# Performance work log

Hardware: AMD Instinct MI355X
Metric: run time of the kernel (lower is better)

The kernel has to match this reference:

```python
import jax, jax.numpy as jnp
import numpy as np

B, T, D, H, FF, TB = 4, 512, 768, 12, 3072, 64
DK = D // H
E = float(np.e)
NEG = -1e9  # stand-in for float('-inf') masked_fill; rows always have valid entries


def layer_norm(x, g, b, eps=1e-5):
    m = jnp.mean(x, axis=-1, keepdims=True)
    v = jnp.mean((x - m) ** 2, axis=-1, keepdims=True)
    return (x - m) * jax.lax.rsqrt(v + eps) * g + b


def setup_inputs() -> dict:
    key = jax.random.key(0)
    ks = jax.random.split(key, 20)
    s = 0.02
    w = lambda k, shape: jax.random.normal(k, shape, jnp.float32) * s
    return {
        "x": jax.random.normal(ks[0], (B, T, D), jnp.float32),
        "batch_temporal_mat": jax.random.uniform(ks[1], (B, T, T), jnp.float32, 0.0, 100.0),
        "padding_masks": jnp.ones((B, 1, T, T), jnp.int32),
        # attention linears (stored (in,out): y = x @ W + b, equals torch x @ W_t.T + b)
        "wq": w(ks[2], (D, D)), "bq": w(ks[3], (D,)),
        "wk": w(ks[4], (D, D)), "bk": w(ks[5], (D,)),
        "wv": w(ks[6], (D, D)), "bv": w(ks[7], (D,)),
        "wp": w(ks[8], (D, D)), "bp": w(ks[9], (D,)),
        # temporal-bias MLP: Linear(1,TB) -> leaky_relu(0.2) -> Linear(TB,1)
        "tb1_w": w(ks[10], (1, TB)), "tb1_b": w(ks[11], (TB,)),
        "tb2_w": w(ks[12], (TB, 1)), "tb2_b": w(ks[13], (1,)),
        # FFN
        "fc1_w": w(ks[14], (D, FF)), "fc1_b": w(ks[15], (FF,)),
        "fc2_w": w(ks[16], (FF, D)), "fc2_b": w(ks[17], (D,)),
        # layernorms
        "ln1_g": jnp.ones((D,), jnp.float32), "ln1_b": jnp.zeros((D,), jnp.float32),
        "ln2_g": jnp.ones((D,), jnp.float32), "ln2_b": jnp.zeros((D,), jnp.float32),
    }


def _block(x, batch_temporal_mat, padding_masks,
           wq, bq, wk, bk, wv, bv, wp, bp,
           tb1_w, tb1_b, tb2_w, tb2_b,
           fc1_w, fc1_b, fc2_w, fc2_b,
           ln1_g, ln1_b, ln2_g, ln2_b):
    # pre-LN attention sublayer
    h = layer_norm(x, ln1_g, ln1_b)
    q = (h @ wq + bq).reshape(B, T, H, DK).transpose(0, 2, 1, 3)  # (B,H,T,DK)
    k = (h @ wk + bk).reshape(B, T, H, DK).transpose(0, 2, 1, 3)
    v = (h @ wv + bv).reshape(B, T, H, DK).transpose(0, 2, 1, 3)
    scores = jnp.einsum('bhid,bhjd->bhij', q, k) * (DK ** -0.5)  # (B,H,T,T)

    # temporal bias: 1/log(e + dt), then per-(i,j) MLP with leaky_relu(0.2)
    tm = 1.0 / jnp.log(E + batch_temporal_mat)                    # (B,T,T)
    hb = jax.nn.leaky_relu(tm[..., None] @ tb1_w + tb1_b, 0.2)    # (B,T,T,TB)
    bias = (hb @ tb2_w + tb2_b)[..., 0]                           # (B,T,T)
    scores = scores + bias[:, None]

    # padding mask then causal (future) mask with CLS row 0 fully visible
    scores = jnp.where(padding_masks == 0, NEG, scores)
    causal = jnp.triu(jnp.ones((T, T), bool), 1).at[0, :].set(False)
    scores = jnp.where(causal, NEG, scores)

    p = jax.nn.softmax(scores, axis=-1)
    out = jnp.einsum('bhij,bhjd->bhid', p, v).transpose(0, 2, 1, 3).reshape(B, T, D)
    out = out @ wp + bp
    x = x + out

    # pre-LN FFN sublayer (exact GELU as in nn.GELU default)
    h2 = layer_norm(x, ln2_g, ln2_b)
    m = jax.nn.gelu(h2 @ fc1_w + fc1_b, approximate=False) @ fc2_w + fc2_b
    return x + m


def reference(x, batch_temporal_mat, padding_masks,
              wq, bq, wk, bk, wv, bv, wp, bp,
              tb1_w, tb1_b, tb2_w, tb2_b,
              fc1_w, fc1_b, fc2_w, fc2_b,
              ln1_g, ln1_b, ln2_g, ln2_b):
    return _block(x, batch_temporal_mat, padding_masks,
                  wq, bq, wk, bk, wv, bv, wp, bp,
                  tb1_w, tb1_b, tb2_w, tb2_b,
                  fc1_w, fc1_b, fc2_w, fc2_b,
                  ln1_g, ln1_b, ln2_g, ln2_b)
```

## Files before the change

### kernel.cpp

```cpp
#include <hip/hip_runtime.h>
#include <hip/hip_bf16.h>
#include <math.h>

#define B_ 4
#define T_ 512
#define D_ 768
#define H_ 12
#define FF_ 3072
#define DK_ 64
#define NTOK (B_*T_)
#define NEGV -1e9f

typedef unsigned short u16;
typedef __bf16 bfx8 __attribute__((ext_vector_type(8)));
typedef float f32x4 __attribute__((ext_vector_type(4)));
typedef u16 u16x8 __attribute__((ext_vector_type(8)));

__device__ __forceinline__ u16 f2bf(float f) {
  union { float f; unsigned u; } v; v.f = f;
  unsigned r = (v.u + 0x7FFFu + ((v.u >> 16) & 1u)) >> 16;
  return (u16)r;
}

__device__ __forceinline__ void glds16(const u16* g, u16* l) {
  __builtin_amdgcn_global_load_lds((const __attribute__((address_space(1))) void*)g,
                                   (__attribute__((address_space(3))) void*)l, 16, 0, 0);
}

__global__ void transpose_all(const float* __restrict__ wq, const float* __restrict__ wk,
                              const float* __restrict__ wv, const float* __restrict__ wp,
                              const float* __restrict__ fc1, const float* __restrict__ fc2,
                              u16* wqT, u16* wkT, u16* wvT, u16* wpT, u16* fc1T, u16* fc2T)
{
  __shared__ float tile[32][33];
  const int bid = blockIdx.x;
  const float* in; u16* outp; int K, N, local;
  if (bid < 2304) {
    int m = bid / 576; local = bid % 576; K = 768; N = 768;
    in   = m == 0 ? wq  : (m == 1 ? wk  : (m == 2 ? wv  : wp));
    outp = m == 0 ? wqT : (m == 1 ? wkT : (m == 2 ? wvT : wpT));
  } else if (bid < 4608) {
    local = bid - 2304; K = 768; N = 3072; in = fc1; outp = fc1T;
  } else {
    local = bid - 4608; K = 3072; N = 768; in = fc2; outp = fc2T;
  }
  const int nt = N / 32;
  const int n0 = (local % nt) * 32, k0 = (local / nt) * 32;
  const int tx = threadIdx.x, ty = threadIdx.y;
  #pragma unroll
  for (int i = 0; i < 4; ++i) {
    int r = ty + i * 8;
    tile[r][tx] = in[(size_t)(k0 + r) * N + n0 + tx];
  }
  __syncthreads();
  #pragma unroll
  for (int i = 0; i < 4; ++i) {
    int r = ty + i * 8;
    outp[(size_t)(n0 + r) * K + k0 + tx] = f2bf(tile[tx][r]);
  }
}

__global__ __launch_bounds__(256) void ln_cast(const float* __restrict__ x, const float* __restrict__ g,
                                               const float* __restrict__ b, u16* __restrict__ out)
{
  const int row = blockIdx.x;
  const int tid = threadIdx.x;
  const float* xr = x + (size_t)row * D_;
  float v0 = xr[tid], v1 = xr[tid + 256], v2 = xr[tid + 512];
  float s = v0 + v1 + v2;
  float sq = v0 * v0 + v1 * v1 + v2 * v2;
  #pragma unroll
  for (int o = 32; o > 0; o >>= 1) { s += __shfl_down(s, o); sq += __shfl_down(sq, o); }
  __shared__ float ss[4], s2[4];
  int w = tid >> 6;
  if ((tid & 63) == 0) { ss[w] = s; s2[w] = sq; }
  __syncthreads();
  s = ss[0] + ss[1] + ss[2] + ss[3];
  sq = s2[0] + s2[1] + s2[2] + s2[3];
  float mean = s * (1.0f / 768.0f);
  float inv = rsqrtf(sq * (1.0f / 768.0f) - mean * mean + 1e-5f);
  u16* orow = out + (size_t)row * D_;
  orow[tid]       = f2bf((v0 - mean) * inv * g[tid]       + b[tid]);
  orow[tid + 256] = f2bf((v1 - mean) * inv * g[tid + 256] + b[tid + 256]);
  orow[tid + 512] = f2bf((v2 - mean) * inv * g[tid + 512] + b[tid + 512]);
}

__global__ __launch_bounds__(256) void bias_mlp(const float* __restrict__ tmat, const int* __restrict__ pad,
    const float* __restrict__ w1, const float* __restrict__ b1,
    const float* __restrict__ w2, const float* __restrict__ b2,
    float* __restrict__ biasM)
{
  __shared__ float sw1[64], sb1[64], sw2[64];
  if (threadIdx.x < 64) {
    sw1[threadIdx.x] = w1[threadIdx.x];
    sb1[threadIdx.x] = b1[threadIdx.x];
    sw2[threadIdx.x] = w2[threadIdx.x];
  }
  __syncthreads();
  size_t idx = (size_t)blockIdx.x * 256 + threadIdx.x;
  float tm = 1.0f / __logf(2.718281828459045f + tmat[idx]);
  float acc = b2[0];
  #pragma unroll
  for (int t = 0; t < 64; ++t) {
    float u = fmaf(tm, sw1[t], sb1[t]);
    u = u > 0.0f ? u : 0.2f * u;
    acc = fmaf(u, sw2[t], acc);
  }
  biasM[idx] = (pad[idx] == 0) ? NEGV : acc;
}

__device__ __forceinline__ void gemm_tile_db(
    const u16* __restrict__ A, const u16* __restrict__ BT,
    int K, int nk, int m0, int n0, int k0,
    u16* As, u16* Bs, f32x4 acc[4][4])
{
  const int tid = threadIdx.x;
  const int w = tid >> 6, lane = tid & 63;
  const int lr = lane & 15, lk = (lane >> 4) * 8;
  const int wm = (w >> 1) * 64, wn = (w & 1) * 64;
  const int c0 = w * 64 + lane, c1 = 256 + c0;
  const int r0 = c0 >> 2, o0 = (c0 & 3) * 8;
  const int r1 = c1 >> 2, o1 = (c1 & 3) * 8;
  const u16* ga0 = A  + (size_t)(m0 + r0) * K + k0 + o0;
  const u16* ga1 = A  + (size_t)(m0 + r1) * K + k0 + o1;
  const u16* gb0 = BT + (size_t)(n0 + r0) * K + k0 + o0;
  const u16* gb1 = BT + (size_t)(n0 + r1) * K + k0 + o1;
  u16* la0 = As + w * 512;
  u16* la1 = As + 2048 + w * 512;
  u16* lb0 = Bs + w * 512;
  u16* lb1 = Bs + 2048 + w * 512;
  glds16(ga0, la0); glds16(ga1, la1); glds16(gb0, lb0); glds16(gb1, lb1);
  __syncthreads();
  int cur = 0;
  for (int kt = 0; kt < nk; ++kt) {
    const int nxt = cur ^ 1;
    if (kt + 1 < nk) {
      ga0 += 32; ga1 += 32; gb0 += 32; gb1 += 32;
      glds16(ga0, la0 + nxt * 4096); glds16(ga1, la1 + nxt * 4096);
      glds16(gb0, lb0 + nxt * 4096); glds16(gb1, lb1 + nxt * 4096);
    }
    const u16* Asc = As + cur * 4096;
    const u16* Bsc = Bs + cur * 4096;
    bfx8 af[4], bfr[4];
    #pragma unroll
    for (int t = 0; t < 4; ++t) {
      af[t]  = *(const bfx8*)&Asc[(wm + t * 16 + lr) * 32 + lk];
      bfr[t] = *(const bfx8*)&Bsc[(wn + t * 16 + lr) * 32 + lk];
    }
    #pragma unroll
    for (int rt = 0; rt < 4; ++rt)
      #pragma unroll
      for (int ct = 0; ct < 4; ++ct)
        acc[rt][ct] = __builtin_amdgcn_mfma_f32_16x16x32_bf16(af[rt], bfr[ct], acc[rt][ct], 0, 0, 0);
    __syncthreads();
    cur = nxt;
  }
}

__global__ __launch_bounds__(256) void gemm_qkv(
    const u16* __restrict__ A,
    const u16* __restrict__ wqT, const u16* __restrict__ wkT, const u16* __restrict__ wvT,
    const float* __restrict__ bq, const float* __restrict__ bk, const float* __restrict__ bv,
    u16* __restrict__ qo, u16* __restrict__ ko, u16* __restrict__ vo)
{
  __shared__ u16 As[2 * 128 * 32];
  __shared__ u16 Bs[2 * 128 * 32];
  const int z = blockIdx.z;
  const u16* BT = z == 0 ? wqT : (z == 1 ? wkT : wvT);
  const float* bias = z == 0 ? bq : (z == 1 ? bk : bv);
  u16* outp = z == 0 ? qo : (z == 1 ? ko : vo);
  const float scale = z == 0 ? 0.125f : 1.0f;
  const int m0 = blockIdx.y * 128, n0 = blockIdx.x * 128;
  f32x4 acc[4][4];
  #pragma unroll
  for (int a = 0; a < 4; ++a)
    #pragma unroll
    for (int bb = 0; bb < 4; ++bb) acc[a][bb] = (f32x4){0.f, 0.f, 0.f, 0.f};
  gemm_tile_db(A, BT, D_, D_ / 32, m0, n0, 0, As, Bs, acc);
  const int tid = threadIdx.x;
  const int w = tid >> 6, lane = tid & 63;
  const int lr = lane & 15;
  const int wm = (w >> 1) * 64, wn = (w & 1) * 64;
  #pragma unroll
  for (int rt = 0; rt < 4; ++rt)
    #pragma unroll
    for (int ct = 0; ct < 4; ++ct)
      #pragma unroll
      for (int r = 0; r < 4; ++r) {
        int m = m0 + wm + rt * 16 + (lane >> 4) * 4 + r;
        int n = n0 + wn + ct * 16 + lr;
        float val = (acc[rt][ct][r] + bias[n]) * scale;
        int b = m >> 9, t = m & 511, hh = n >> 6, d = n & 63;
        if (z < 2) outp[(((size_t)b * H_ + hh) * T_ + t) * DK_ + d] = f2bf(val);
        else       outp[(((size_t)b * H_ + hh) * DK_ + d) * T_ + t] = f2bf(val);
      }
}

__global__ __launch_bounds__(256) void gemm_part(
    const u16* __restrict__ A, const u16* __restrict__ BT,
    float* __restrict__ part, int M, int N, int K, int Ksplit)
{
  __shared__ u16 As[2 * 128 * 32];
  __shared__ u16 Bs[2 * 128 * 32];
  const int m0 = blockIdx.y * 128, n0 = blockIdx.x * 128;
  const int kz = blockIdx.z;
  f32x4 acc[4][4];
  #pragma unroll
  for (int a = 0; a < 4; ++a)
    #pragma unroll
    for (int bb = 0; bb < 4; ++bb) acc[a][bb] = (f32x4){0.f, 0.f, 0.f, 0.f};
  gemm_tile_db(A, BT, K, Ksplit / 32, m0, n0, kz * Ksplit, As, Bs, acc);
  const int tid = threadIdx.x;
  const int w = tid >> 6, lane = tid & 63;
  const int lr = lane & 15;
  const int wm = (w >> 1) * 64, wn = (w & 1) * 64;
  float* pp = part + (size_t)kz * M * N;
  #pragma unroll
  for (int rt = 0; rt < 4; ++rt)
    #pragma unroll
    for (int ct = 0; ct < 4; ++ct)
      #pragma unroll
      for (int r = 0; r < 4; ++r) {
        int m = m0 + wm + rt * 16 + (lane >> 4) * 4 + r;
        int n = n0 + wn + ct * 16 + lr;
        pp[(size_t)m * N + n] = acc[rt][ct][r];
      }
}

__global__ __launch_bounds__(256) void gemm_gelu(
    const u16* __restrict__ A, const u16* __restrict__ BT,
    const float* __restrict__ bias, u16* __restrict__ outp, int M, int N, int K)
{
  __shared__ u16 As[2 * 128 * 32];
  __shared__ u16 Bs[2 * 128 * 32];
  const int m0 = blockIdx.y * 128, n0 = blockIdx.x * 128;
  f32x4 acc[4][4];
  #pragma unroll
  for (int a = 0; a < 4; ++a)
    #pragma unroll
    for (int bb = 0; bb < 4; ++bb) acc[a][bb] = (f32x4){0.f, 0.f, 0.f, 0.f};
  gemm_tile_db(A, BT, K, K / 32, m0, n0, 0, As, Bs, acc);
  const int tid = threadIdx.x;
  const int w = tid >> 6, lane = tid & 63;
  const int lr = lane & 15;
  const int wm = (w >> 1) * 64, wn = (w & 1) * 64;
  #pragma unroll
  for (int rt = 0; rt < 4; ++rt)
    #pragma unroll
    for (int ct = 0; ct < 4; ++ct)
      #pragma unroll
      for (int r = 0; r < 4; ++r) {
        int m = m0 + wm + rt * 16 + (lane >> 4) * 4 + r;
        int n = n0 + wn + ct * 16 + lr;
        float val = acc[rt][ct][r] + bias[n];
        float gl = 0.5f * val * (1.0f + erff(val * 0.7071067811865475f));
        outp[(size_t)m * N + n] = f2bf(gl);
      }
}

__global__ __launch_bounds__(256) void reduce_ln(
    const float* __restrict__ part, const float* __restrict__ x, const float* __restrict__ bp,
    const float* __restrict__ g, const float* __restrict__ bta,
    float* __restrict__ x1, u16* __restrict__ h2)
{
  const int row = blockIdx.x;
  const int tid = threadIdx.x;
  const size_t base = (size_t)row * D_;
  const size_t slab = (size_t)NTOK * D_;
  float v[3];
  float s = 0.f, sq = 0.f;
  #pragma unroll
  for (int i = 0; i < 3; ++i) {
    int c = tid + i * 256;
    float val = x[base + c] + bp[c] + part[base + c] + part[slab + base + c];
    v[i] = val;
    s += val; sq += val * val;
  }
  #pragma unroll
  for (int o = 32; o > 0; o >>= 1) { s += __shfl_down(s, o); sq += __shfl_down(sq, o); }
  __shared__ float ss[4], s2[4];
  int w = tid >> 6;
  if ((tid & 63) == 0) { ss[w] = s; s2[w] = sq; }
  __syncthreads();
  s = ss[0] + ss[1] + ss[2] + ss[3];
  sq = s2[0] + s2[1] + s2[2] + s2[3];
  float mean = s * (1.0f / 768.0f);
  float inv = rsqrtf(sq * (1.0f / 768.0f) - mean * mean + 1e-5f);
  #pragma unroll
  for (int i = 0; i < 3; ++i) {
    int c = tid + i * 256;
    x1[base + c] = v[i];
    h2[base + c] = f2bf((v[i] - mean) * inv * g[c] + bta[c]);
  }
}

__global__ __launch_bounds__(256) void reduce_out(
    const float* __restrict__ part, const float* __restrict__ x1,
    const float* __restrict__ bias, float* __restrict__ out)
{
  const size_t i = (size_t)blockIdx.x * 256 + threadIdx.x;
  const size_t slab = (size_t)NTOK * D_ / 4;
  float4 b = ((const float4*)bias)[i % (D_ / 4)];
  float4 a = ((const float4*)x1)[i];
  float4 p0 = ((const float4*)part)[i];
  float4 p1 = ((const float4*)part)[i + slab];
  float4 p2 = ((const float4*)part)[i + 2 * slab];
  float4 p3 = ((const float4*)part)[i + 3 * slab];
  float4 o;
  o.x = a.x + b.x + p0.x + p1.x + p2.x + p3.x;
  o.y = a.y + b.y + p0.y + p1.y + p2.y + p3.y;
  o.z = a.z + b.z + p0.z + p1.z + p2.z + p3.z;
  o.w = a.w + b.w + p0.w + p1.w + p2.w + p3.w;
  ((float4*)out)[i] = o;
}

__global__ __launch_bounds__(256) void attn_kernel(
    const u16* __restrict__ q, const u16* __restrict__ k, const u16* __restrict__ vT,
    const float* __restrict__ biasM, u16* __restrict__ ao)
{
  __shared__ u16 P[16 * 512];
  __shared__ float pmax[64], psum[64];
  const int tid = threadIdx.x;
  const int w = tid >> 6, lane = tid & 63;
  const int lr = lane & 15, hi = lane >> 4, lk = hi * 8;

  const int bid = blockIdx.x;
  const int xcd = bid & 7, idx = bid >> 3;
  const int bh = xcd * 6 + (idx >> 5);
  const int i0 = (idx & 31) * 16;
  const int b = bh / H_, h = bh % H_;
  const int tmax = (i0 == 0) ? 31 : ((i0 >> 4) + 1);
  const int nks  = (i0 == 0) ? 16 : ((i0 >> 5) + 1);

  bfx8 qf[2];
  #pragma unroll
  for (int ks = 0; ks < 2; ++ks)
    qf[ks] = *(const bfx8*)(q + ((size_t)bh * T_ + i0 + lr) * DK_ + ks * 32 + lk);
  f32x4 acc[8];
  float mx[4] = {-3.4e38f, -3.4e38f, -3.4e38f, -3.4e38f};
  #pragma unroll
  for (int ct = 0; ct < 8; ++ct) {
    const int t = ct * 4 + w;
    if (t > tmax) continue;
    const int j0 = t * 16;
    bfx8 kf0 = *(const bfx8*)(k + ((size_t)bh * T_ + j0 + lr) * DK_ + lk);
    bfx8 kf1 = *(const bfx8*)(k + ((size_t)bh * T_ + j0 + lr) * DK_ + 32 + lk);
    f32x4 a0 = (f32x4){0.f, 0.f, 0.f, 0.f};
    a0 = __builtin_amdgcn_mfma_f32_16x16x32_bf16(qf[0], kf0, a0, 0, 0, 0);
    a0 = __builtin_amdgcn_mfma_f32_16x16x32_bf16(qf[1], kf1, a0, 0, 0, 0);
    const int j = j0 + lr;
    #pragma unroll
    for (int r = 0; r < 4; ++r) {
      int i = i0 + hi * 4 + r;
      float s = a0[r] + biasM[((size_t)b * T_ + i) * T_ + j];
      if (j > i && i != 0) s = NEGV;
      a0[r] = s;
      mx[r] = fmaxf(mx[r], s);
    }
    acc[ct] = a0;
  }
  #pragma unroll
  for (int o = 1; o < 16; o <<= 1)
    #pragma unroll
    for (int r = 0; r < 4; ++r) mx[r] = fmaxf(mx[r], __shfl_xor(mx[r], o));
  if (lr == 0) {
    #pragma unroll
    for (int r = 0; r < 4; ++r) pmax[w * 16 + hi * 4 + r] = mx[r];
  }
  __syncthreads();

  float sm[4] = {0.f, 0.f, 0.f, 0.f};
  float M[4];
  #pragma unroll
  for (int r = 0; r < 4; ++r) {
    int row = hi * 4 + r;
    M[r] = fmaxf(fmaxf(pmax[row], pmax[16 + row]), fmaxf(pmax[32 + row], pmax[48 + row]));
  }
  char* Pb = (char*)P;
  #pragma unroll
  for (int ct = 0; ct < 8; ++ct) {
    const int t = ct * 4 + w;
    if (t > tmax) continue;
    const int col = t * 16 + lr;
    #pragma unroll
    for (int r = 0; r < 4; ++r) {
      float p = __expf(acc[ct][r] - M[r]);
      sm[r] += p;
      int row = hi * 4 + r;
      int byte = (row * 1024 + col * 2) ^ ((row & 7) << 4);
      *(u16*)(Pb + byte) = f2bf(p);
    }
  }
  #pragma unroll
  for (int o = 1; o < 16; o <<= 1)
    #pragma unroll
    for (int r = 0; r < 4; ++r) sm[r] += __shfl_xor(sm[r], o);
  if (lr == 0) {
    #pragma unroll
    for (int r = 0; r < 4; ++r) psum[w * 16 + hi * 4 + r] = sm[r];
  }
  __syncthreads();

  float rinv[4];
  #pragma unroll
  for (int r = 0; r < 4; ++r) {
    int row = hi * 4 + r;
    rinv[r] = 1.0f / (psum[row] + psum[16 + row] + psum[32 + row] + psum[48 + row]);
  }

  {
    const int n0 = w * 16;
    f32x4 oacc = (f32x4){0.f, 0.f, 0.f, 0.f};
    for (int ks = 0; ks < nks; ++ks) {
      int byte = (lr * 1024 + (ks * 32 + lk) * 2) ^ ((lr & 7) << 4);
      bfx8 pa = *(const bfx8*)(Pb + byte);
      bfx8 vf = *(const bfx8*)(vT + ((size_t)bh * DK_ + n0 + lr) * T_ + ks * 32 + lk);
      oacc = __builtin_amdgcn_mfma_f32_16x16x32_bf16(pa, vf, oacc, 0, 0, 0);
    }
    #pragma unroll
    for (int r = 0; r < 4; ++r) {
      int i = i0 + hi * 4 + r;
      ao[((size_t)b * T_ + i) * D_ + h * DK_ + n0 + lr] = f2bf(oacc[r] * rinv[r]);
    }
  }
}

extern "C" void kernel_launch(void* const* d_in, const int* in_sizes, int n_in,
                              void* d_out, int out_size, void* d_ws, size_t ws_size,
                              hipStream_t stream) {
  (void)in_sizes; (void)n_in; (void)out_size; (void)ws_size;
  const float* x    = (const float*)d_in[0];
  const float* tmat = (const float*)d_in[1];
  const int*   pad  = (const int*)d_in[2];
  const float* wq = (const float*)d_in[3];  const float* bq = (const float*)d_in[4];
  const float* wk = (const float*)d_in[5];  const float* bk = (const float*)d_in[6];
  const float* wv = (const float*)d_in[7];  const float* bv = (const float*)d_in[8];
  const float* wp = (const float*)d_in[9];  const float* bp = (const float*)d_in[10];
  const float* tb1w = (const float*)d_in[11]; const float* tb1b = (const float*)d_in[12];
  const float* tb2w = (const float*)d_in[13]; const float* tb2b = (const float*)d_in[14];
  const float* fc1w = (const float*)d_in[15]; const float* fc1b = (const float*)d_in[16];
  const float* fc2w = (const float*)d_in[17]; const float* fc2b = (const float*)d_in[18];
  const float* ln1g = (const float*)d_in[19]; const float* ln1b = (const float*)d_in[20];
  const float* ln2g = (const float*)d_in[21]; const float* ln2b = (const float*)d_in[22];
  float* out = (float*)d_out;

  char* p = (char*)d_ws;
  u16* wqT  = (u16*)p; p += (size_t)768 * 768 * 2;
  u16* wkT  = (u16*)p; p += (size_t)768 * 768 * 2;
  u16* wvT  = (u16*)p; p += (size_t)768 * 768 * 2;
  u16* wpT  = (u16*)p; p += (size_t)768 * 768 * 2;
  u16* fc1T = (u16*)p; p += (size_t)768 * 3072 * 2;
  u16* fc2T = (u16*)p; p += (size_t)3072 * 768 * 2;
  float* x1 = (float*)p; p += (size_t)NTOK * D_ * 4;
  u16* gbuf = (u16*)p; p += (size_t)NTOK * FF_ * 2;
  char* pool = p;
  u16*   hbuf  = (u16*)(pool + 0);
  u16*   qb    = (u16*)(pool + 3145728);
  u16*   kb    = (u16*)(pool + 6291456);
  u16*   vTb   = (u16*)(pool + 9437184);
  float* biasM = (float*)(pool + 12582912);
  u16*   ao    = (u16*)(pool + 16777216);
  u16*   h2    = (u16*)(pool + 19922944);
  float* partP = (float*)(pool + 0);
  float* partF = (float*)(pool + 0);

  transpose_all<<<6912, dim3(32, 8), 0, stream>>>(wq, wk, wv, wp, fc1w, fc2w,
                                                  wqT, wkT, wvT, wpT, fc1T, fc2T);
  ln_cast<<<NTOK, 256, 0, stream>>>(x, ln1g, ln1b, hbuf);
  bias_mlp<<<(B_ * T_ * T_) / 256, 256, 0, stream>>>(tmat, pad, tb1w, tb1b, tb2w, tb2b, biasM);

  gemm_qkv<<<dim3(6, 16, 3), 256, 0, stream>>>(hbuf, wqT, wkT, wvT, bq, bk, bv, qb, kb, vTb);
  attn_kernel<<<1536, 256, 0, stream>>>(qb, kb, vTb, biasM, ao);

  gemm_part<<<dim3(6, 16, 2), 256, 0, stream>>>(ao, wpT, partP, NTOK, 768, 768, 384);
  reduce_ln<<<NTOK, 256, 0, stream>>>(partP, x, bp, ln2g, ln2b, x1, h2);

  gemm_gelu<<<dim3(24, 16), 256, 0, stream>>>(h2, fc1T, fc1b, gbuf, NTOK, FF_, 768);

  gemm_part<<<dim3(6, 16, 4), 256, 0, stream>>>(gbuf, fc2T, partF, NTOK, 768, 3072, 768);
  reduce_out<<<NTOK * D_ / 4 / 256, 256, 0, stream>>>(partF, x1, fc2b, out);
}
```

Before: 153.1 us.

## Merge prep kernels, triple-buffer GEMM loads, and process 32 query rows per attention block

Combines the weight transpose, LN1 cast and temporal-bias MLP into a single launch. Replaces the double-buffered GEMM K-loop with a three-stage ring that keeps two tiles in flight, using explicit vmcnt waits and one barrier per iteration. Changes the attention kernel so each block handles 32 query rows instead of 16, reusing the K and V fragments across two row groups and halving the grid. This raises LDS use and register pressure, which may reduce occupancy.

```diff
diff --git a/kernel.cpp b/kernel.cpp
--- a/kernel.cpp
+++ b/kernel.cpp
@@ -27,89 +27,88 @@
                                    (__attribute__((address_space(3))) void*)l, 16, 0, 0);
 }
 
-__global__ void transpose_all(const float* __restrict__ wq, const float* __restrict__ wk,
-                              const float* __restrict__ wv, const float* __restrict__ wp,
-                              const float* __restrict__ fc1, const float* __restrict__ fc2,
-                              u16* wqT, u16* wkT, u16* wvT, u16* wpT, u16* fc1T, u16* fc2T)
-{
-  __shared__ float tile[32][33];
+__global__ __launch_bounds__(256) void prep_kernel(
+    const float* __restrict__ x,
+    const float* __restrict__ wq, const float* __restrict__ wk,
+    const float* __restrict__ wv, const float* __restrict__ wp,
+    const float* __restrict__ fc1, const float* __restrict__ fc2,
+    u16* wqT, u16* wkT, u16* wvT, u16* wpT, u16* fc1T, u16* fc2T,
+    const float* __restrict__ ln1g, const float* __restrict__ ln1b, u16* __restrict__ hbuf,
+    const float* __restrict__ tmat, const int* __restrict__ pad,
+    const float* __restrict__ tb1w, const float* __restrict__ tb1b,
+    const float* __restrict__ tb2w, const float* __restrict__ tb2b,
+    float* __restrict__ biasM)
+{
   const int bid = blockIdx.x;
-  const float* in; u16* outp; int K, N, local;
-  if (bid < 2304) {
-    int m = bid / 576; local = bid % 576; K = 768; N = 768;
-    in   = m == 0 ? wq  : (m == 1 ? wk  : (m == 2 ? wv  : wp));
-    outp = m == 0 ? wqT : (m == 1 ? wkT : (m == 2 ? wvT : wpT));
-  } else if (bid < 4608) {
-    local = bid - 2304; K = 768; N = 3072; in = fc1; outp = fc1T;
+  const int tid = threadIdx.x;
+  if (bid < 6912) {
+    __shared__ float tile[32][33];
+    const float* in; u16* outp; int K, N, local;
+    if (bid < 2304) {
+      int m = bid / 576; local = bid % 576; K = 768; N = 768;
+      in   = m == 0 ? wq  : (m == 1 ? wk  : (m == 2 ? wv  : wp));
+      outp = m == 0 ? wqT : (m == 1 ? wkT : (m == 2 ? wvT : wpT));
+    } else if (bid < 4608) {
+      local = bid - 2304; K = 768; N = 3072; in = fc1; outp = fc1T;
+    } else {
+      local = bid - 4608; K = 3072; N = 768; in = fc2; outp = fc2T;
+    }
+    const int nt = N / 32;
+    const int n0 = (local % nt) * 32, k0 = (local / nt) * 32;
+    const int tx = tid & 31, ty = tid >> 5;
+    #pragma unroll
+    for (int i = 0; i < 4; ++i) {
+      int r = ty + i * 8;
+      tile[r][tx] = in[(size_t)(k0 + r) * N + n0 + tx];
+    }
+    __syncthreads();
+    #pragma unroll
+    for (int i = 0; i < 4; ++i) {
+      int r = ty + i * 8;
+      outp[(size_t)(n0 + r) * K + k0 + tx] = f2bf(tile[tx][r]);
+    }
+  } else if (bid < 8960) {
+    const int row = bid - 6912;
+    const float* xr = x + (size_t)row * D_;
+    float v0 = xr[tid], v1 = xr[tid + 256], v2 = xr[tid + 512];
+    float s = v0 + v1 + v2;
+    float sq = v0 * v0 + v1 * v1 + v2 * v2;
+    #pragma unroll
+    for (int o = 32; o > 0; o >>= 1) { s += __shfl_down(s, o); sq += __shfl_down(sq, o); }
+    __shared__ float ss[4], s2[4];
+    int w = tid >> 6;
+    if ((tid & 63) == 0) { ss[w] = s; s2[w] = sq; }
+    __syncthreads();
+    s = ss[0] + ss[1] + ss[2] + ss[3];
+    sq = s2[0] + s2[1] + s2[2] + s2[3];
+    float mean = s * (1.0f / 768.0f);
+    float inv = rsqrtf(sq * (1.0f / 768.0f) - mean * mean + 1e-5f);
+    u16* orow = hbuf + (size_t)row * D_;
+    orow[tid]       = f2bf((v0 - mean) * inv * ln1g[tid]       + ln1b[tid]);
+    orow[tid + 256] = f2bf((v1 - mean) * inv * ln1g[tid + 256] + ln1b[tid + 256]);
+    orow[tid + 512] = f2bf((v2 - mean) * inv * ln1g[tid + 512] + ln1b[tid + 512]);
   } else {
-    local = bid - 4608; K = 3072; N = 768; in = fc2; outp = fc2T;
-  }
-  const int nt = N / 32;
-  const int n0 = (local % nt) * 32, k0 = (local / nt) * 32;
-  const int tx = threadIdx.x, ty = threadIdx.y;
-  #pragma unroll
-  for (int i = 0; i < 4; ++i) {
-    int r = ty + i * 8;
-    tile[r][tx] = in[(size_t)(k0 + r) * N + n0 + tx];
-  }
-  __syncthreads();
-  #pragma unroll
-  for (int i = 0; i < 4; ++i) {
-    int r = ty + i * 8;
-    outp[(size_t)(n0 + r) * K + k0 + tx] = f2bf(tile[tx][r]);
-  }
-}
-
-__global__ __launch_bounds__(256) void ln_cast(const float* __restrict__ x, const float* __restrict__ g,
-                                               const float* __restrict__ b, u16* __restrict__ out)
-{
-  const int row = blockIdx.x;
-  const int tid = threadIdx.x;
-  const float* xr = x + (size_t)row * D_;
-  float v0 = xr[tid], v1 = xr[tid + 256], v2 = xr[tid + 512];
-  float s = v0 + v1 + v2;
-  float sq = v0 * v0 + v1 * v1 + v2 * v2;
-  #pragma unroll
-  for (int o = 32; o > 0; o >>= 1) { s += __shfl_down(s, o); sq += __shfl_down(sq, o); }
-  __shared__ float ss[4], s2[4];
-  int w = tid >> 6;
-  if ((tid & 63) == 0) { ss[w] = s; s2[w] = sq; }
-  __syncthreads();
-  s = ss[0] + ss[1] + ss[2] + ss[3];
-  sq = s2[0] + s2[1] + s2[2] + s2[3];
-  float mean = s * (1.0f / 768.0f);
-  float inv = rsqrtf(sq * (1.0f / 768.0f) - mean * mean + 1e-5f);
-  u16* orow = out + (size_t)row * D_;
-  orow[tid]       = f2bf((v0 - mean) * inv * g[tid]       + b[tid]);
-  orow[tid + 256] = f2bf((v1 - mean) * inv * g[tid + 256] + b[tid + 256]);
-  orow[tid + 512] = f2bf((v2 - mean) * inv * g[tid + 512] + b[tid + 512]);
-}
-
-__global__ __launch_bounds__(256) void bias_mlp(const float* __restrict__ tmat, const int* __restrict__ pad,
-    const float* __restrict__ w1, const float* __restrict__ b1,
-    const float* __restrict__ w2, const float* __restrict__ b2,
-    float* __restrict__ biasM)
-{
-  __shared__ float sw1[64], sb1[64], sw2[64];
-  if (threadIdx.x < 64) {
-    sw1[threadIdx.x] = w1[threadIdx.x];
-    sb1[threadIdx.x] = b1[threadIdx.x];
-    sw2[threadIdx.x] = w2[threadIdx.x];
-  }
-  __syncthreads();
-  size_t idx = (size_t)blockIdx.x * 256 + threadIdx.x;
-  float tm = 1.0f / __logf(2.718281828459045f + tmat[idx]);
-  float acc = b2[0];
-  #pragma unroll
-  for (int t = 0; t < 64; ++t) {
-    float u = fmaf(tm, sw1[t], sb1[t]);
-    u = u > 0.0f ? u : 0.2f * u;
-    acc = fmaf(u, sw2[t], acc);
-  }
-  biasM[idx] = (pad[idx] == 0) ? NEGV : acc;
-}
-
-__device__ __forceinline__ void gemm_tile_db(
+    __shared__ float sw1[64], sb1[64], sw2[64];
+    if (tid < 64) {
+      sw1[tid] = tb1w[tid];
+      sb1[tid] = tb1b[tid];
+      sw2[tid] = tb2w[tid];
+    }
+    __syncthreads();
+    size_t idx = (size_t)(bid - 8960) * 256 + tid;
+    float tm = 1.0f / __logf(2.718281828459045f + tmat[idx]);
+    float acc = tb2b[0];
+    #pragma unroll
+    for (int t = 0; t < 64; ++t) {
+      float u = fmaf(tm, sw1[t], sb1[t]);
+      u = u > 0.0f ? u : 0.2f * u;
+      acc = fmaf(u, sw2[t], acc);
+    }
+    biasM[idx] = (pad[idx] == 0) ? NEGV : acc;
+  }
+}
+
+__device__ __forceinline__ void gemm_tile_p2(
     const u16* __restrict__ A, const u16* __restrict__ BT,
     int K, int nk, int m0, int n0, int k0,
     u16* As, u16* Bs, f32x4 acc[4][4])
@@ -121,26 +120,30 @@
   const int c0 = w * 64 + lane, c1 = 256 + c0;
   const int r0 = c0 >> 2, o0 = (c0 & 3) * 8;
   const int r1 = c1 >> 2, o1 = (c1 & 3) * 8;
-  const u16* ga0 = A  + (size_t)(m0 + r0) * K + k0 + o0;
-  const u16* ga1 = A  + (size_t)(m0 + r1) * K + k0 + o1;
-  const u16* gb0 = BT + (size_t)(n0 + r0) * K + k0 + o0;
-  const u16* gb1 = BT + (size_t)(n0 + r1) * K + k0 + o1;
+  const u16* gA0 = A  + (size_t)(m0 + r0) * K + k0 + o0;
+  const u16* gA1 = A  + (size_t)(m0 + r1) * K + k0 + o1;
+  const u16* gB0 = BT + (size_t)(n0 + r0) * K + k0 + o0;
+  const u16* gB1 = BT + (size_t)(n0 + r1) * K + k0 + o1;
   u16* la0 = As + w * 512;
   u16* la1 = As + 2048 + w * 512;
   u16* lb0 = Bs + w * 512;
   u16* lb1 = Bs + 2048 + w * 512;
-  glds16(ga0, la0); glds16(ga1, la1); glds16(gb0, lb0); glds16(gb1, lb1);
-  __syncthreads();
-  int cur = 0;
+#define ISSUE_TILE(kk, b) do { \
+    glds16(gA0 + (size_t)(kk) * 32, la0 + (b) * 4096); \
+    glds16(gA1 + (size_t)(kk) * 32, la1 + (b) * 4096); \
+    glds16(gB0 + (size_t)(kk) * 32, lb0 + (b) * 4096); \
+    glds16(gB1 + (size_t)(kk) * 32, lb1 + (b) * 4096); } while (0)
+  ISSUE_TILE(0, 0);
+  if (nk > 1) ISSUE_TILE(1, 1);
+  int cb = 0;
   for (int kt = 0; kt < nk; ++kt) {
-    const int nxt = cur ^ 1;
-    if (kt + 1 < nk) {
-      ga0 += 32; ga1 += 32; gb0 += 32; gb1 += 32;
-      glds16(ga0, la0 + nxt * 4096); glds16(ga1, la1 + nxt * 4096);
-      glds16(gb0, lb0 + nxt * 4096); glds16(gb1, lb1 + nxt * 4096);
-    }
-    const u16* Asc = As + cur * 4096;
-    const u16* Bsc = Bs + cur * 4096;
+    if (kt < nk - 2) asm volatile("s_waitcnt vmcnt(4)" ::: "memory");
+    else             asm volatile("s_waitcnt vmcnt(0)" ::: "memory");
+    __builtin_amdgcn_sched_barrier(0);
+    __builtin_amdgcn_s_barrier();
+    __builtin_amdgcn_sched_barrier(0);
+    const u16* Asc = As + cb * 4096;
+    const u16* Bsc = Bs + cb * 4096;
     bfx8 af[4], bfr[4];
     #pragma unroll
     for (int t = 0; t < 4; ++t) {
@@ -152,9 +155,13 @@
       #pragma unroll
       for (int ct = 0; ct < 4; ++ct)
         acc[rt][ct] = __builtin_amdgcn_mfma_f32_16x16x32_bf16(af[rt], bfr[ct], acc[rt][ct], 0, 0, 0);
-    __syncthreads();
-    cur = nxt;
-  }
+    if (kt + 2 < nk) {
+      int nb = cb + 2; if (nb >= 3) nb -= 3;
+      ISSUE_TILE(kt + 2, nb);
+    }
+    cb = cb + 1; if (cb >= 3) cb = 0;
+  }
+#undef ISSUE_TILE
 }
 
 __global__ __launch_bounds__(256) void gemm_qkv(
@@ -163,8 +170,8 @@
     const float* __restrict__ bq, const float* __restrict__ bk, const float* __restrict__ bv,
     u16* __restrict__ qo, u16* __restrict__ ko, u16* __restrict__ vo)
 {
-  __shared__ u16 As[2 * 128 * 32];
-  __shared__ u16 Bs[2 * 128 * 32];
+  __shared__ u16 As[3 * 128 * 32];
+  __shared__ u16 Bs[3 * 128 * 32];
   const int z = blockIdx.z;
   const u16* BT = z == 0 ? wqT : (z == 1 ? wkT : wvT);
   const float* bias = z == 0 ? bq : (z == 1 ? bk : bv);
@@ -176,7 +183,7 @@
   for (int a = 0; a < 4; ++a)
     #pragma unroll
     for (int bb = 0; bb < 4; ++bb) acc[a][bb] = (f32x4){0.f, 0.f, 0.f, 0.f};
-  gemm_tile_db(A, BT, D_, D_ / 32, m0, n0, 0, As, Bs, acc);
+  gemm_tile_p2(A, BT, D_, D_ / 32, m0, n0, 0, As, Bs, acc);
   const int tid = threadIdx.x;
   const int w = tid >> 6, lane = tid & 63;
   const int lr = lane & 15;
@@ -200,8 +207,8 @@
     const u16* __restrict__ A, const u16* __restrict__ BT,
     float* __restrict__ part, int M, int N, int K, int Ksplit)
 {
-  __shared__ u16 As[2 * 128 * 32];
-  __shared__ u16 Bs[2 * 128 * 32];
+  __shared__ u16 As[3 * 128 * 32];
+  __shared__ u16 Bs[3 * 128 * 32];
   const int m0 = blockIdx.y * 128, n0 = blockIdx.x * 128;
   const int kz = blockIdx.z;
   f32x4 acc[4][4];
@@ -209,7 +216,7 @@
   for (int a = 0; a < 4; ++a)
     #pragma unroll
     for (int bb = 0; bb < 4; ++bb) acc[a][bb] = (f32x4){0.f, 0.f, 0.f, 0.f};
-  gemm_tile_db(A, BT, K, Ksplit / 32, m0, n0, kz * Ksplit, As, Bs, acc);
+  gemm_tile_p2(A, BT, K, Ksplit / 32, m0, n0, kz * Ksplit, As, Bs, acc);
   const int tid = threadIdx.x;
   const int w = tid >> 6, lane = tid & 63;
   const int lr = lane & 15;
@@ -231,15 +238,15 @@
     const u16* __restrict__ A, const u16* __restrict__ BT,
     const float* __restrict__ bias, u16* __restrict__ outp, int M, int N, int K)
 {
-  __shared__ u16 As[2 * 128 * 32];
-  __shared__ u16 Bs[2 * 128 * 32];
+  __shared__ u16 As[3 * 128 * 32];
+  __shared__ u16 Bs[3 * 128 * 32];
   const int m0 = blockIdx.y * 128, n0 = blockIdx.x * 128;
   f32x4 acc[4][4];
   #pragma unroll
   for (int a = 0; a < 4; ++a)
     #pragma unroll
     for (int bb = 0; bb < 4; ++bb) acc[a][bb] = (f32x4){0.f, 0.f, 0.f, 0.f};
-  gemm_tile_db(A, BT, K, K / 32, m0, n0, 0, As, Bs, acc);
+  gemm_tile_p2(A, BT, K, K / 32, m0, n0, 0, As, Bs, acc);
   const int tid = threadIdx.x;
   const int w = tid >> 6, lane = tid & 63;
   const int lr = lane & 15;
@@ -318,26 +325,32 @@
     const u16* __restrict__ q, const u16* __restrict__ k, const u16* __restrict__ vT,
     const float* __restrict__ biasM, u16* __restrict__ ao)
 {
-  __shared__ u16 P[16 * 512];
-  __shared__ float pmax[64], psum[64];
+  __shared__ u16 P[32 * 512];
+  __shared__ float pmax[128], psum[128];
   const int tid = threadIdx.x;
   const int w = tid >> 6, lane = tid & 63;
   const int lr = lane & 15, hi = lane >> 4, lk = hi * 8;
 
   const int bid = blockIdx.x;
   const int xcd = bid & 7, idx = bid >> 3;
-  const int bh = xcd * 6 + (idx >> 5);
-  const int i0 = (idx & 31) * 16;
+  const int bh = xcd * 6 + (idx >> 4);
+  const int i0 = (idx & 15) * 32;
   const int b = bh / H_, h = bh % H_;
   const int tmax = (i0 == 0) ? 31 : ((i0 >> 4) + 1);
   const int nks  = (i0 == 0) ? 16 : ((i0 >> 5) + 1);
 
-  bfx8 qf[2];
-  #pragma unroll
-  for (int ks = 0; ks < 2; ++ks)
-    qf[ks] = *(const bfx8*)(q + ((size_t)bh * T_ + i0 + lr) * DK_ + ks * 32 + lk);
-  f32x4 acc[8];
-  float mx[4] = {-3.4e38f, -3.4e38f, -3.4e38f, -3.4e38f};
+  bfx8 qf[2][2];
+  #pragma unroll
+  for (int g = 0; g < 2; ++g)
+    #pragma unroll
+    for (int ks = 0; ks < 2; ++ks)
+      qf[g][ks] = *(const bfx8*)(q + ((size_t)bh * T_ + i0 + g * 16 + lr) * DK_ + ks * 32 + lk);
+  f32x4 acc[8][2];
+  float mx[2][4];
+  #pragma unroll
+  for (int g = 0; g < 2; ++g)
+    #pragma unroll
+    for (int r = 0; r < 4; ++r) mx[g][r] = -3.4e38f;
   #pragma unroll
   for (int ct = 0; ct < 8; ++ct) {
     const int t = ct * 4 + w;
@@ -345,37 +358,46 @@
     const int j0 = t * 16;
     bfx8 kf0 = *(const bfx8*)(k + ((size_t)bh * T_ + j0 + lr) * DK_ + lk);
     bfx8 kf1 = *(const bfx8*)(k + ((size_t)bh * T_ + j0 + lr) * DK_ + 32 + lk);
-    f32x4 a0 = (f32x4){0.f, 0.f, 0.f, 0.f};
-    a0 = __builtin_amdgcn_mfma_f32_16x16x32_bf16(qf[0], kf0, a0, 0, 0, 0);
-    a0 = __builtin_amdgcn_mfma_f32_16x16x32_bf16(qf[1], kf1, a0, 0, 0, 0);
     const int j = j0 + lr;
     #pragma unroll
+    for (int g = 0; g < 2; ++g) {
+      f32x4 a0 = (f32x4){0.f, 0.f, 0.f, 0.f};
+      a0 = __builtin_amdgcn_mfma_f32_16x16x32_bf16(qf[g][0], kf0, a0, 0, 0, 0);
+      a0 = __builtin_amdgcn_mfma_f32_16x16x32_bf16(qf[g][1], kf1, a0, 0, 0, 0);
+      #pragma unroll
+      for (int r = 0; r < 4; ++r) {
+        int i = i0 + g * 16 + hi * 4 + r;
+        float s = a0[r] + biasM[((size_t)b * T_ + i) * T_ + j];
+        if (j > i && i != 0) s = NEGV;
+        a0[r] = s;
+        mx[g][r] = fmaxf(mx[g][r], s);
+      }
+      acc[ct][g] = a0;
+    }
+  }
+  #pragma unroll
+  for (int o = 1; o < 16; o <<= 1)
+    #pragma unroll
+    for (int g = 0; g < 2; ++g)
+      #pragma unroll
+      for (int r = 0; r < 4; ++r) mx[g][r] = fmaxf(mx[g][r], __shfl_xor(mx[g][r], o));
+  if (lr == 0) {
+    #pragma unroll
+    for (int g = 0; g < 2; ++g)
+      #pragma unroll
+      for (int r = 0; r < 4; ++r) pmax[w * 32 + g * 16 + hi * 4 + r] = mx[g][r];
+  }
+  __syncthreads();
+
+  float M2[2][4], sm[2][4];
+  #pragma unroll
+  for (int g = 0; g < 2; ++g)
+    #pragma unroll
     for (int r = 0; r < 4; ++r) {
-      int i = i0 + hi * 4 + r;
-      float s = a0[r] + biasM[((size_t)b * T_ + i) * T_ + j];
-      if (j > i && i != 0) s = NEGV;
-      a0[r] = s;
-      mx[r] = fmaxf(mx[r], s);
-    }
-    acc[ct] = a0;
-  }
-  #pragma unroll
-  for (int o = 1; o < 16; o <<= 1)
-    #pragma unroll
-    for (int r = 0; r < 4; ++r) mx[r] = fmaxf(mx[r], __shfl_xor(mx[r], o));
-  if (lr == 0) {
-    #pragma unroll
-    for (int r = 0; r < 4; ++r) pmax[w * 16 + hi * 4 + r] = mx[r];
-  }
-  __syncthreads();
-
-  float sm[4] = {0.f, 0.f, 0.f, 0.f};
-  float M[4];
-  #pragma unroll
-  for (int r = 0; r < 4; ++r) {
-    int row = hi * 4 + r;
-    M[r] = fmaxf(fmaxf(pmax[row], pmax[16 + row]), fmaxf(pmax[32 + row], pmax[48 + row]));
-  }
+      int row = g * 16 + hi * 4 + r;
+      M2[g][r] = fmaxf(fmaxf(pmax[row], pmax[32 + row]), fmaxf(pmax[64 + row], pmax[96 + row]));
+      sm[g][r] = 0.f;
+    }
   char* Pb = (char*)P;
   #pragma unroll
   for (int ct = 0; ct < 8; ++ct) {
@@ -383,44 +405,61 @@
     if (t > tmax) continue;
     const int col = t * 16 + lr;
     #pragma unroll
+    for (int g = 0; g < 2; ++g)
+      #pragma unroll
+      for (int r = 0; r < 4; ++r) {
+        float pexp = __expf(acc[ct][g][r] - M2[g][r]);
+        sm[g][r] += pexp;
+        int row = g * 16 + hi * 4 + r;
+        int byte = (row * 1024 + col * 2) ^ ((row & 7) << 4);
+        *(u16*)(Pb + byte) = f2bf(pexp);
+      }
+  }
+  #pragma unroll
+  for (int o = 1; o < 16; o <<= 1)
+    #pragma unroll
+    for (int g = 0; g < 2; ++g)
+      #pragma unroll
+      for (int r = 0; r < 4; ++r) sm[g][r] += __shfl_xor(sm[g][r], o);
+  if (lr == 0) {
+    #pragma unroll
+    for (int g = 0; g < 2; ++g)
+      #pragma unroll
+      for (int r = 0; r < 4; ++r) psum[w * 32 + g * 16 + hi * 4 + r] = sm[g][r];
+  }
+  __syncthreads();
+
+  float rinv[2][4];
+  #pragma unroll
+  for (int g = 0; g < 2; ++g)
+    #pragma unroll
     for (int r = 0; r < 4; ++r) {
-      float p = __expf(acc[ct][r] - M[r]);
-      sm[r] += p;
-      int row = hi * 4 + r;
-      int byte = (row * 1024 + col * 2) ^ ((row & 7) << 4);
-      *(u16*)(Pb + byte) = f2bf(p);
-    }
-  }
-  #pragma unroll
-  for (int o = 1; o < 16; o <<= 1)
-    #pragma unroll
-    for (int r = 0; r < 4; ++r) sm[r] += __shfl_xor(sm[r], o);
-  if (lr == 0) {
-    #pragma unroll
-    for (int r = 0; r < 4; ++r) psum[w * 16 + hi * 4 + r] = sm[r];
-  }
-  __syncthreads();
-
-  float rinv[4];
-  #pragma unroll
-  for (int r = 0; r < 4; ++r) {
-    int row = hi * 4 + r;
-    rinv[r] = 1.0f / (psum[row] + psum[16 + row] + psum[32 + row] + psum[48 + row]);
-  }
+      int row = g * 16 + hi * 4 + r;
+      rinv[g][r] = 1.0f / (psum[row] + psum[32 + row] + psum[64 + row] + psum[96 + row]);
+    }
 
   {
     const int n0 = w * 16;
-    f32x4 oacc = (f32x4){0.f, 0.f, 0.f, 0.f};
+    f32x4 oa0 = (f32x4){0.f, 0.f, 0.f, 0.f};
+    f32x4 oa1 = (f32x4){0.f, 0.f, 0.f, 0.f};
     for (int ks = 0; ks < nks; ++ks) {
-      int byte = (lr * 1024 + (ks * 32 + lk) * 2) ^ ((lr & 7) << 4);
-      bfx8 pa = *(const bfx8*)(Pb + byte);
       bfx8 vf = *(const bfx8*)(vT + ((size_t)bh * DK_ + n0 + lr) * T_ + ks * 32 + lk);
-      oacc = __builtin_amdgcn_mfma_f32_16x16x32_bf16(pa, vf, oacc, 0, 0, 0);
+      int byte0 = (lr * 1024 + (ks * 32 + lk) * 2) ^ ((lr & 7) << 4);
+      int byte1 = ((16 + lr) * 1024 + (ks * 32 + lk) * 2) ^ ((lr & 7) << 4);
+      bfx8 pa0 = *(const bfx8*)(Pb + byte0);
+      bfx8 pa1 = *(const bfx8*)(Pb + byte1);
+      oa0 = __builtin_amdgcn_mfma_f32_16x16x32_bf16(pa0, vf, oa0, 0, 0, 0);
+      oa1 = __builtin_amdgcn_mfma_f32_16x16x32_bf16(pa1, vf, oa1, 0, 0, 0);
     }
     #pragma unroll
     for (int r = 0; r < 4; ++r) {
       int i = i0 + hi * 4 + r;
-      ao[((size_t)b * T_ + i) * D_ + h * DK_ + n0 + lr] = f2bf(oacc[r] * rinv[r]);
+      ao[((size_t)b * T_ + i) * D_ + h * DK_ + n0 + lr] = f2bf(oa0[r] * rinv[0][r]);
+    }
+    #pragma unroll
+    for (int r = 0; r < 4; ++r) {
+      int i = i0 + 16 + hi * 4 + r;
+      ao[((size_t)b * T_ + i) * D_ + h * DK_ + n0 + lr] = f2bf(oa1[r] * rinv[1][r]);
     }
   }
 }
@@ -464,13 +503,13 @@
   float* partP = (float*)(pool + 0);
   float* partF = (float*)(pool + 0);
 
-  transpose_all<<<6912, dim3(32, 8), 0, stream>>>(wq, wk, wv, wp, fc1w, fc2w,
-                                                  wqT, wkT, wvT, wpT, fc1T, fc2T);
-  ln_cast<<<NTOK, 256, 0, stream>>>(x, ln1g, ln1b, hbuf);
-  bias_mlp<<<(B_ * T_ * T_) / 256, 256, 0, stream>>>(tmat, pad, tb1w, tb1b, tb2w, tb2b, biasM);
+  prep_kernel<<<13056, 256, 0, stream>>>(x, wq, wk, wv, wp, fc1w, fc2w,
+                                         wqT, wkT, wvT, wpT, fc1T, fc2T,
+                                         ln1g, ln1b, hbuf,
+                                         tmat, pad, tb1w, tb1b, tb2w, tb2b, biasM);
 
   gemm_qkv<<<dim3(6, 16, 3), 256, 0, stream>>>(hbuf, wqT, wkT, wvT, bq, bk, bv, qb, kb, vTb);
-  attn_kernel<<<1536, 256, 0, stream>>>(qb, kb, vTb, biasM, ao);
+  attn_kernel<<<768, 256, 0, stream>>>(qb, kb, vTb, biasM, ao);
 
   gemm_part<<<dim3(6, 16, 2), 256, 0, stream>>>(ao, wpT, partP, NTOK, 768, 768, 384);
   reduce_ln<<<NTOK, 256, 0, stream>>>(partP, x, bp, ln2g, ln2b, x1, h2);
```

Result: faster. 139.4 us (-8.9%).
